# Optimization experiments

Hardware: AMD Instinct MI355X
Metric: run time of the kernel (lower is better)

Reference implementation:

```python
import jax, jax.numpy as jnp
import numpy as np

VOCAB, DIM, NC, KS, NCLASS = 50000, 300, 256, 3, 3
B, L1, L2 = 128, 512, 32
PAD = (KS - 1) // 2


def setup_inputs() -> dict:
    key = jax.random.key(0)
    ks = jax.random.split(key, 12)
    return {
        "context_ids": jax.random.randint(ks[0], (B, L1), 0, VOCAB),
        "context_masks": jnp.ones((B, L1), jnp.float32),
        "aspect_ids": jax.random.randint(ks[1], (B, L2), 0, VOCAB),
        "aspect_masks": jnp.ones((B, L2), jnp.float32),
        "wordmat": jax.random.normal(ks[2], (VOCAB, DIM), jnp.float32) * 0.1,
        "W": jax.random.normal(ks[3], (DIM, DIM), jnp.float32) * (2.0 / DIM) ** 0.5,
        "ctx_w": jax.random.normal(ks[4], (NC, DIM, KS), jnp.float32) * 0.02,
        "ctx_b": jnp.zeros((NC,), jnp.float32),
        "gate_w": jax.random.normal(ks[5], (NC, 2 * DIM, KS), jnp.float32) * 0.02,
        "gate_b": jnp.zeros((NC,), jnp.float32),
        "lin_w": jax.random.normal(ks[6], (NCLASS, NC), jnp.float32) * 0.05,
        "lin_b": jnp.zeros((NCLASS,), jnp.float32),
    }


def masked_softmax(A, mask):
    # A: (b, l1, l2); mask: (b, l2); normalize over dim=1 (l1), faithful to source
    A_max = jnp.max(A, axis=1, keepdims=True)
    A_exp = jnp.exp(A - A_max) * mask[:, None, :]
    return A_exp / (jnp.sum(A_exp, axis=1, keepdims=True) + 1e-10)


def conv1d(x, w, b):
    # x: (B, C_in, L), w: (C_out, C_in, K) -> (B, C_out, L)
    y = jax.lax.conv_general_dilated(x, w, (1,), [(PAD, PAD)],
                                     dimension_numbers=("NCH", "OIH", "NCH"))
    return y + b[None, :, None]


def reference(context_ids, context_masks, aspect_ids, aspect_masks,
              wordmat, W, ctx_w, ctx_b, gate_w, gate_b, lin_w, lin_b):
    context = wordmat[context_ids]          # (B, L1, D)
    aspect = wordmat[aspect_ids]            # (B, L2, D)
    # FullyAwareAttention
    sx = jax.nn.relu(jnp.einsum("bld,de->ble", context, W))
    sy = jax.nn.relu(jnp.einsum("bld,de->ble", aspect, W))
    s = jnp.einsum("bie,bje->bij", sx, sy)  # (B, L1, L2)
    alpha = masked_softmax(s, aspect_masks)
    att = jnp.einsum("bij,bjd->bid", alpha, aspect)  # (B, L1, D)
    gate_input = jnp.concatenate([context, att], axis=-1)  # (B, L1, 2D)
    sentiment = jnp.tanh(conv1d(context.transpose(0, 2, 1), ctx_w, ctx_b))
    gate = jax.nn.relu(conv1d(gate_input.transpose(0, 2, 1), gate_w, gate_b))
    out = jnp.max(sentiment * gate, axis=2)  # global maxpool over length
    return out @ lin_w.T + lin_b
```

## Files before the change

### kernel.cpp

```cpp
#include <hip/hip_runtime.h>
#include <hip/hip_bf16.h>
#include <math.h>
#include <stdint.h>

#define DIM 300
#define NC 256
#define KS 3
#define NCLASS 3
#define BB 128
#define L1 512
#define L2 32

#define XW 352
#define XROWS 514
#define ROW_B (XW * 2)
#define NKC 11
#define WP2_ELEMS (2 * 4 * 10 * 3 * 4 * 64 * 8)
#define WB_ELEMS (10 * 19 * 64 * 8)
#define WG2_ELEMS (3 * 10 * 16 * 64 * 8)
#define GT_ELEMS (BB * 3 * 32 * 256)
#define GP_ELEMS (BB * 2 * 2 * 3 * 4 * 64 * 8)
#define GP_B_STRIDE (2 * 2 * 3 * 4 * 64 * 8)
#define WAVE_WP_B (10 * 3 * 4 * 1024)

#define ABUF_B 4224
#define EP_LD 260

typedef __attribute__((ext_vector_type(8))) short bf16x8;
typedef __attribute__((ext_vector_type(4))) short bf16x4;
typedef __attribute__((ext_vector_type(4))) float f32x4;

#define GLOBAL_AS __attribute__((address_space(1)))
#define LDS_AS __attribute__((address_space(3)))

__device__ __forceinline__ void gload_lds16(const void* g, void* l) {
    __builtin_amdgcn_global_load_lds((const GLOBAL_AS void*)g, (LDS_AS void*)l, 16, 0, 0);
}

static __device__ __forceinline__ short bfr(float x) {
    __hip_bfloat16 h = __float2bfloat16(x);
    return *(short*)&h;
}

__global__ void prep_wp(const float* __restrict__ ctx_w,
                        const float* __restrict__ gate_w,
                        __hip_bfloat16* __restrict__ Wp2) {
    int idx = blockIdx.x * 256 + threadIdx.x;
    if (idx >= WP2_ELEMS) return;
    int jj = idx & 7;
    int lane = (idx >> 3) & 63;
    int n = (idx >> 9) & 3;
    int rest = idx >> 11;
    int tap = rest % 3;
    int r2 = rest / 3;
    int kc = r2 % 10;
    int w = r2 / 10;
    int role = w & 3, cbv = w >> 2;
    int k = kc * 32 + ((lane >> 4) << 3) + jj;
    int nl = role * 64 + n * 16 + (lane & 15);
    float v = 0.f;
    if (nl < 128) {
        int ch = cbv * 128 + nl;
        if (k < 300) v = ctx_w[(ch * DIM + k) * KS + tap];
    } else {
        int ch = cbv * 128 + (nl - 128);
        if (k < 300) v = gate_w[(ch * 2 * DIM + k) * KS + tap];
    }
    Wp2[idx] = __float2bfloat16(v);
}

__global__ void prep_wb(const float* __restrict__ Wm,
                        __hip_bfloat16* __restrict__ Wb) {
    int idx = blockIdx.x * 256 + threadIdx.x;
    if (idx >= WB_ELEMS) return;
    int j = idx & 7;
    int l = (idx >> 3) & 63;
    int r = idx >> 9;
    int nf = r % 19, kc = r / 19;
    int k = kc * 32 + ((l >> 4) << 3) + j;
    int n = nf * 16 + (l & 15);
    float v = (k < 300 && n < 300) ? Wm[k * DIM + n] : 0.f;
    Wb[idx] = __float2bfloat16(v);
}

__global__ void prep_wg2(const float* __restrict__ gate_w,
                         __hip_bfloat16* __restrict__ Wg2) {
    int idx = blockIdx.x * 256 + threadIdx.x;
    if (idx >= WG2_ELEMS) return;
    int jj = idx & 7;
    int lane = (idx >> 3) & 63;
    int rest = idx >> 9;
    int nf = rest % 16;
    int r2 = rest / 16;
    int kc = r2 % 10, tap = r2 / 10;
    int k = kc * 32 + ((lane >> 4) << 3) + jj;
    int n = nf * 16 + (lane & 15);
    float v = (k < 300) ? gate_w[(n * 2 * DIM + DIM + k) * KS + tap] : 0.f;
    Wg2[idx] = __float2bfloat16(v);
}

__global__ void gather_rows(const int* __restrict__ ids,
                            const float* __restrict__ wordmat,
                            __hip_bfloat16* __restrict__ aspb,
                            __hip_bfloat16* __restrict__ syb) {
    int row = blockIdx.x;
    int id = ids[row];
    const float* src = wordmat + (size_t)id * DIM;
    for (int d = threadIdx.x; d < 320; d += blockDim.x) {
        if (d < DIM) {
            aspb[(size_t)row * 320 + d] = __float2bfloat16(src[d]);
        } else {
            aspb[(size_t)row * 320 + d] = __float2bfloat16(0.f);
            if (d >= 304) syb[(size_t)row * 320 + d] = __float2bfloat16(0.f);
        }
    }
}

__global__ __launch_bounds__(256, 2) void prep_g(
        const __hip_bfloat16* __restrict__ aspb,
        const __hip_bfloat16* __restrict__ Wg2,
        __hip_bfloat16* __restrict__ Gt) {
    const int t = threadIdx.x, wave = t >> 6, l = t & 63;
    const int lane15 = l & 15, lq = l >> 4;
    const int b = blockIdx.x, tap = blockIdx.y;
    f32x4 acc[2][4];
    #pragma unroll
    for (int m = 0; m < 2; ++m)
        #pragma unroll
        for (int ni = 0; ni < 4; ++ni) acc[m][ni] = (f32x4)0.f;
    const char* Ab = (const char*)aspb + (size_t)b * 32 * 640;
    const bf16x8* WgV = (const bf16x8*)Wg2;
    for (int kc = 0; kc < 10; ++kc) {
        bf16x8 af[2];
        #pragma unroll
        for (int m = 0; m < 2; ++m)
            af[m] = *(const bf16x8*)(Ab + (size_t)(m * 16 + lane15) * 640 + kc * 64 + lq * 16);
        #pragma unroll
        for (int ni = 0; ni < 4; ++ni) {
            bf16x8 bw = WgV[((size_t)(tap * 10 + kc) * 16 + wave * 4 + ni) * 64 + l];
            #pragma unroll
            for (int m = 0; m < 2; ++m)
                acc[m][ni] = __builtin_amdgcn_mfma_f32_16x16x32_bf16(af[m], bw, acc[m][ni], 0, 0, 0);
        }
    }
    #pragma unroll
    for (int m = 0; m < 2; ++m)
        #pragma unroll
        for (int ni = 0; ni < 4; ++ni) {
            int c = (wave * 4 + ni) * 16 + lane15;
            #pragma unroll
            for (int i2 = 0; i2 < 4; ++i2) {
                int j = m * 16 + lq * 4 + i2;
                Gt[((size_t)(b * 3 + tap) * 32 + j) * 256 + c] = __float2bfloat16(acc[m][ni][i2]);
            }
        }
}

__global__ void prep_gp(const __hip_bfloat16* __restrict__ Gt,
                        __hip_bfloat16* __restrict__ Gp) {
    int idx = blockIdx.x * 256 + threadIdx.x;
    if (idx >= GP_ELEMS) return;
    int jj = idx & 7;
    int lane = (idx >> 3) & 63;
    int nf = (idx >> 9) & 3;
    int rest = idx >> 11;
    int tap = rest % 3;
    int r2 = rest / 3;
    int gr = r2 & 1, cbv = (r2 >> 1) & 1, b = r2 >> 2;
    int j = ((lane >> 4) << 3) + jj;
    int c = cbv * 128 + gr * 64 + nf * 16 + (lane & 15);
    Gp[idx] = Gt[((size_t)(b * 3 + tap) * 32 + j) * 256 + c];
}

__global__ __launch_bounds__(256) void xcat_x(const int* __restrict__ cids,
                                              const float* __restrict__ wordmat,
                                              __hip_bfloat16* __restrict__ Xc) {
    int t = threadIdx.x;
    int rloc = t >> 5, lane = t & 31;
    int row = blockIdx.x * 8 + rloc;
    int b = row >> 9, l = row & 511;
    size_t id = (size_t)cids[row];
    const float4* src = (const float4*)(wordmat + id * DIM);
    __hip_bfloat16* dst = Xc + ((size_t)b * XROWS + 1 + l) * XW;
    #pragma unroll
    for (int c = lane; c < 80; c += 32) {
        bf16x4 o;
        if (c < 75) {
            float4 f = src[c];
            o[0] = bfr(f.x); o[1] = bfr(f.y); o[2] = bfr(f.z); o[3] = bfr(f.w);
        } else {
            o = (bf16x4)0;
        }
        ((bf16x4*)dst)[c] = o;
    }
    if (blockIdx.x < 256 && t < 88) {
        int b2 = blockIdx.x >> 1;
        int gr = (blockIdx.x & 1) ? (XROWS - 1) : 0;
        ((bf16x4*)(Xc + ((size_t)b2 * XROWS + gr) * XW))[t] = (bf16x4)0;
    }
}

__global__ __launch_bounds__(256, 2) void sy_mfma(
        const __hip_bfloat16* __restrict__ aspb,
        const __hip_bfloat16* __restrict__ Wb,
        __hip_bfloat16* __restrict__ syb) {
    const int t = threadIdx.x, wave = t >> 6, l = t & 63;
    const int lane15 = l & 15, lq = l >> 4;
    const int g = blockIdx.x * 64 + wave * 16 + lane15;
    f32x4 acc[19];
    #pragma unroll
    for (int nf = 0; nf < 19; ++nf) acc[nf] = (f32x4)0.f;
    const bf16x8* Arow = (const bf16x8*)((const char*)aspb + (size_t)g * 640);
    const bf16x8* WbV = (const bf16x8*)Wb;
    for (int kc = 0; kc < 10; ++kc) {
        bf16x8 af = Arow[kc * 4 + lq];
        #pragma unroll
        for (int nf = 0; nf < 19; ++nf)
            acc[nf] = __builtin_amdgcn_mfma_f32_16x16x32_bf16(
                af, WbV[(kc * 19 + nf) * 64 + l], acc[nf], 0, 0, 0);
    }
    #pragma unroll
    for (int nf = 0; nf < 19; ++nf) {
        int col = nf * 16 + lane15;
        #pragma unroll
        for (int i2 = 0; i2 < 4; ++i2) {
            int row = blockIdx.x * 64 + wave * 16 + lq * 4 + i2;
            syb[(size_t)row * 320 + col] = __float2bfloat16(fmaxf(acc[nf][i2], 0.f));
        }
    }
}

__global__ __launch_bounds__(256, 2) void sxs_mfma(
        const __hip_bfloat16* __restrict__ Xc,
        const __hip_bfloat16* __restrict__ Wb,
        const __hip_bfloat16* __restrict__ syb,
        float* __restrict__ s) {
    __shared__ __align__(16) char sxL[4 * 16 * 640];
    const int t = threadIdx.x, wave = t >> 6, l = t & 63;
    const int lane15 = l & 15, lq = l >> 4;
    const int lb = blockIdx.x, b = blockIdx.y;
    const int g = b * XROWS + 1 + lb * 64 + wave * 16 + lane15;

    f32x4 acc[19];
    #pragma unroll
    for (int nf = 0; nf < 19; ++nf) acc[nf] = (f32x4)0.f;

    const bf16x8* Arow = (const bf16x8*)((const char*)Xc + (size_t)g * ROW_B);
    const bf16x8* WbV = (const bf16x8*)Wb;
    for (int kc = 0; kc < 10; ++kc) {
        bf16x8 af = Arow[kc * 4 + lq];
        #pragma unroll
        for (int nf = 0; nf < 19; ++nf)
            acc[nf] = __builtin_amdgcn_mfma_f32_16x16x32_bf16(
                af, WbV[(kc * 19 + nf) * 64 + l], acc[nf], 0, 0, 0);
    }

    char* sxW = sxL + wave * (16 * 640);
    if (l < 32) {
        int row = l >> 1;
        int phys = (2 + (l & 1)) ^ ((row >> 2) & 3);
        *(f32x4*)(sxW + row * 640 + 576 + phys * 16) = (f32x4)0.f;
    }
    #pragma unroll
    for (int nf = 0; nf < 19; ++nf) {
        int col = nf * 16 + lane15;
        #pragma unroll
        for (int i2 = 0; i2 < 4; ++i2) {
            int row = lq * 4 + i2;
            int off = row * 640 + ((col >> 5) << 6) +
                      ((((col >> 3) & 3) ^ ((row >> 2) & 3)) << 4) + ((col & 7) << 1);
            *(__hip_bfloat16*)(sxW + off) = __float2bfloat16(fmaxf(acc[nf][i2], 0.f));
        }
    }
    f32x4 acc2[2];
    acc2[0] = (f32x4)0.f;
    acc2[1] = (f32x4)0.f;
    const bf16x8* syV = (const bf16x8*)syb + (size_t)b * 32 * 40;
    for (int kc = 0; kc < 10; ++kc) {
        bf16x8 af2 = *(const bf16x8*)(sxW + lane15 * 640 + kc * 64 +
                                      ((lq ^ ((lane15 >> 2) & 3)) << 4));
        #pragma unroll
        for (int nj = 0; nj < 2; ++nj) {
            bf16x8 bfj = syV[(nj * 16 + lane15) * 40 + kc * 4 + lq];
            acc2[nj] = __builtin_amdgcn_mfma_f32_16x16x32_bf16(af2, bfj, acc2[nj], 0, 0, 0);
        }
    }
    #pragma unroll
    for (int nj = 0; nj < 2; ++nj)
        #pragma unroll
        for (int i2 = 0; i2 < 4; ++i2) {
            int i = lb * 64 + wave * 16 + lq * 4 + i2;
            s[((size_t)b * L1 + i) * L2 + nj * 16 + lane15] = acc2[nj][i2];
        }
}

__global__ __launch_bounds__(256) void softmax_col(const float* __restrict__ s,
                                                   const float* __restrict__ amask,
                                                   __hip_bfloat16* __restrict__ Xc) {
    __shared__ float red[256];
    __shared__ float cmax[16], cscale[16];
    int b = blockIdx.x, jh = blockIdx.y, t = threadIdx.x;
    int jl = t & 15, j = jh * 16 + jl, ii = t >> 4;
    const float* sb = s + (size_t)b * L1 * L2;
    float v[32];
    float m = -1e30f;
    #pragma unroll
    for (int q = 0; q < 32; ++q) {
        v[q] = sb[(size_t)(ii + q * 16) * L2 + j];
        m = fmaxf(m, v[q]);
    }
    red[t] = m;
    __syncthreads();
    if (t < 16) {
        float mm = red[t];
        for (int p = 1; p < 16; ++p) mm = fmaxf(mm, red[p * 16 + t]);
        cmax[t] = mm;
    }
    __syncthreads();
    float cm = cmax[jl];
    float sum = 0.f;
    #pragma unroll
    for (int q = 0; q < 32; ++q) {
        v[q] = expf(v[q] - cm);
        sum += v[q];
    }
    red[t] = sum;
    __syncthreads();
    if (t < 16) {
        float ss = 0.f;
        for (int p = 0; p < 16; ++p) ss += red[p * 16 + t];
        float mk = amask[b * L2 + jh * 16 + t];
        cscale[t] = mk / (mk * ss + 1e-10f);
    }
    __syncthreads();
    float sc = cscale[jl];
    #pragma unroll
    for (int q = 0; q < 32; ++q) {
        int row = ii + q * 16;
        Xc[((size_t)b * XROWS + 1 + row) * XW + 320 + j] = __float2bfloat16(v[q] * sc);
    }
}

__global__ __launch_bounds__(256, 4) void conv_mfma(
        const __hip_bfloat16* __restrict__ Xc,
        const __hip_bfloat16* __restrict__ Wp2,
        const __hip_bfloat16* __restrict__ Gp,
        const float* __restrict__ ctx_b,
        const float* __restrict__ gate_b,
        float* __restrict__ part) {
    __shared__ __align__(16) char lds[16 * EP_LD * 4];
    const int t = threadIdx.x, wave = t >> 6, lane = t & 63;
    const int lane15 = lane & 15, lq = lane >> 4;
    const int lb = blockIdx.x >> 1, cb = blockIdx.x & 1;
    const int b = blockIdx.y, l0 = lb * 64;
    const int role = wave ^ ((blockIdx.x & 1) << 1);

    f32x4 acc[4][4];
    #pragma unroll
    for (int m = 0; m < 4; ++m)
        #pragma unroll
        for (int n = 0; n < 4; ++n) acc[m][n] = (f32x4)0.f;

    const char* XcB = (const char*)Xc + ((size_t)b * XROWS + l0) * ROW_B;
    const char* bbase = (const char*)Wp2 + (size_t)(cb * 4 + role) * WAVE_WP_B + lane * 16;
    const char* gbase = (const char*)Gp + ((size_t)b * GP_B_STRIDE +
                        (size_t)(cb * 2 + (role & 1)) * (3 * 4 * 512)) * 2 + lane * 16;

    #define STAGE_A(kc_, buf_) do {                                              \
        char* Ab_ = lds + (buf_) * ABUF_B;                                       \
        _Pragma("unroll")                                                        \
        for (int i = 0; i < 2; ++i) {                                            \
            int chunk = (i * 4 + wave) * 64 + lane;                              \
            if (chunk < 264) {                                                   \
                int row_ = chunk >> 2, c_ = chunk & 3;                           \
                int sc_ = (c_ ^ ((row_ >> 1) & 3)) << 4;                         \
                gload_lds16(XcB + (size_t)row_ * ROW_B + (kc_) * 64 + sc_,       \
                            Ab_ + (i * 4 + wave) * 1024);                        \
            }                                                                    \
        }                                                                        \
    } while (0)

    STAGE_A(0, 0);
    __syncthreads();

    for (int kc = 0; kc < NKC; ++kc) {
        const int cbuf = kc & 1;
        if (kc < NKC - 1) STAGE_A(kc + 1, cbuf ^ 1);
        if (kc < 10 || role >= 2) {
            const char* Ab = lds + cbuf * ABUF_B;
            #pragma unroll
            for (int tap = 0; tap < 3; ++tap) {
                bf16x8 bw[4];
                #pragma unroll
                for (int n = 0; n < 4; ++n)
                    bw[n] = (kc < 10)
                        ? *(const bf16x8*)(bbase + (size_t)((kc * 3 + tap) * 4 + n) * 1024)
                        : *(const bf16x8*)(gbase + (size_t)(tap * 4 + n) * 1024);
                bf16x8 af[4];
                #pragma unroll
                for (int m = 0; m < 4; ++m) {
                    int row = m * 16 + lane15 + tap;
                    af[m] = *(const bf16x8*)(Ab + row * 64 +
                                             ((lq ^ ((row >> 1) & 3)) << 4));
                }
                #pragma unroll
                for (int m = 0; m < 4; ++m)
                    #pragma unroll
                    for (int n = 0; n < 4; ++n)
                        acc[m][n] = __builtin_amdgcn_mfma_f32_16x16x32_bf16(
                            af[m], bw[n], acc[m][n], 0, 0, 0);
            }
        }
        __syncthreads();
    }
    #undef STAGE_A

    const int c0 = cb * 128;
    const int cl = t & 127, rh = t >> 7;
    const float bs = ctx_b[c0 + cl];
    const float bg = gate_b[c0 + cl];
    float* ep = (float*)lds;
    float pm = -1e30f;
    for (int ms = 0; ms < 4; ++ms) {
        __syncthreads();
        #pragma unroll
        for (int n = 0; n < 4; ++n) {
            int col = (role << 6) + (n << 4) + lane15;
            #pragma unroll
            for (int i2 = 0; i2 < 4; ++i2)
                ep[(lq * 4 + i2) * EP_LD + col] = acc[ms][n][i2];
        }
        __syncthreads();
        #pragma unroll
        for (int rr = 0; rr < 8; ++rr) {
            int r = rh * 8 + rr;
            float sv = ep[r * EP_LD + cl] + bs;
            float gv = ep[r * EP_LD + 128 + cl] + bg;
            pm = fmaxf(pm, tanhf(sv) * fmaxf(gv, 0.f));
        }
    }
    __syncthreads();
    ep[t] = pm;
    __syncthreads();
    if (t < 128)
        part[((size_t)b * 8 + lb) * 256 + c0 + cl] = fmaxf(ep[t], ep[t + 128]);
}

__global__ __launch_bounds__(256) void finalize(const float* __restrict__ part,
                                                const float* __restrict__ lin_w,
                                                const float* __restrict__ lin_b,
                                                float* __restrict__ out) {
    __shared__ float pl[256];
    __shared__ float red[256];
    int b = blockIdx.x, t = threadIdx.x;
    float p = part[((size_t)b * 8) * 256 + t];
    for (int lb = 1; lb < 8; ++lb)
        p = fmaxf(p, part[((size_t)b * 8 + lb) * 256 + t]);
    pl[t] = p;
    __syncthreads();
    for (int n = 0; n < NCLASS; ++n) {
        red[t] = pl[t] * lin_w[n * NC + t];
        __syncthreads();
        for (int sft = 128; sft > 0; sft >>= 1) {
            if (t < sft) red[t] += red[t + sft];
            __syncthreads();
        }
        if (t == 0) out[b * NCLASS + n] = red[0] + lin_b[n];
        __syncthreads();
    }
}

extern "C" void kernel_launch(void* const* d_in, const int* in_sizes, int n_in,
                              void* d_out, int out_size, void* d_ws, size_t ws_size,
                              hipStream_t stream) {
    const int* cids = (const int*)d_in[0];
    const int* aids = (const int*)d_in[2];
    const float* amask = (const float*)d_in[3];
    const float* wordmat = (const float*)d_in[4];
    const float* Wm = (const float*)d_in[5];
    const float* ctx_w = (const float*)d_in[6];
    const float* ctx_b = (const float*)d_in[7];
    const float* gate_w = (const float*)d_in[8];
    const float* gate_b = (const float*)d_in[9];
    const float* lin_w = (const float*)d_in[10];
    const float* lin_b = (const float*)d_in[11];
    float* out = (float*)d_out;

    float* sbuf = (float*)d_ws;
    float* part = sbuf + 2097152;
    __hip_bfloat16* aspb = (__hip_bfloat16*)(part + 262144);
    __hip_bfloat16* sybf = aspb + 1310720;
    __hip_bfloat16* Wb   = sybf + 1310720;
    __hip_bfloat16* Wp2  = Wb + WB_ELEMS;
    __hip_bfloat16* Wg2  = Wp2 + WP2_ELEMS;
    __hip_bfloat16* Gt   = Wg2 + WG2_ELEMS;
    __hip_bfloat16* Gp   = Gt + GT_ELEMS;
    __hip_bfloat16* Xc   = Gp + GP_ELEMS;

    prep_wp<<<(WP2_ELEMS + 255) / 256, 256, 0, stream>>>(ctx_w, gate_w, Wp2);
    prep_wb<<<(WB_ELEMS + 255) / 256, 256, 0, stream>>>(Wm, Wb);
    prep_wg2<<<(WG2_ELEMS + 255) / 256, 256, 0, stream>>>(gate_w, Wg2);
    gather_rows<<<BB * L2, 256, 0, stream>>>(aids, wordmat, aspb, sybf);
    xcat_x<<<BB * L1 / 8, 256, 0, stream>>>(cids, wordmat, Xc);
    sy_mfma<<<(BB * L2) / 64, 256, 0, stream>>>(aspb, Wb, sybf);
    prep_g<<<dim3(BB, 3), 256, 0, stream>>>(aspb, Wg2, Gt);
    prep_gp<<<(GP_ELEMS + 255) / 256, 256, 0, stream>>>(Gt, Gp);
    sxs_mfma<<<dim3(L1 / 64, BB), 256, 0, stream>>>(Xc, Wb, sybf, sbuf);
    softmax_col<<<dim3(BB, 2), 256, 0, stream>>>(sbuf, amask, Xc);
    conv_mfma<<<dim3(16, BB), 256, 0, stream>>>(Xc, Wp2, Gp, ctx_b, gate_b, part);
    finalize<<<BB, 256, 0, stream>>>(part, lin_w, lin_b, out);
}
```

Before: 195.5 us.

## Merge prep kernels, drop Gp repack, widen conv blocks to 512 threads

Folds the three weight-prep kernels and the aspect gather into one launch, and merges the sy projection and the G precompute into one kernel. The Gp repack kernel is removed; the gate waves now read Gt directly with scalar 2-byte gathers. Conv blocks become 512 threads covering all 256 channels, so each staged X tile is shared by both channel halves. Softmax is split over 4 column groups for more parallelism. These changes cut launch overhead and duplicated X loads, at the cost of uncoalesced Gt reads and higher per-block register and LDS pressure.

New measurement: 171.6 us. 1.14x faster.

```diff
diff --git a/kernel.cpp b/kernel.cpp
--- a/kernel.cpp
+++ b/kernel.cpp
@@ -19,12 +19,11 @@
 #define WB_ELEMS (10 * 19 * 64 * 8)
 #define WG2_ELEMS (3 * 10 * 16 * 64 * 8)
 #define GT_ELEMS (BB * 3 * 32 * 256)
-#define GP_ELEMS (BB * 2 * 2 * 3 * 4 * 64 * 8)
-#define GP_B_STRIDE (2 * 2 * 3 * 4 * 64 * 8)
+#define GATH_ELEMS (BB * L2 * 320)
 #define WAVE_WP_B (10 * 3 * 4 * 1024)
 
 #define ABUF_B 4224
-#define EP_LD 260
+#define EP_LD 516
 
 typedef __attribute__((ext_vector_type(8))) short bf16x8;
 typedef __attribute__((ext_vector_type(4))) short bf16x4;
@@ -42,134 +41,76 @@
     return *(short*)&h;
 }
 
-__global__ void prep_wp(const float* __restrict__ ctx_w,
-                        const float* __restrict__ gate_w,
-                        __hip_bfloat16* __restrict__ Wp2) {
+__global__ void prep_all(const float* __restrict__ ctx_w,
+                         const float* __restrict__ gate_w,
+                         const float* __restrict__ Wm,
+                         const int* __restrict__ aids,
+                         const float* __restrict__ wordmat,
+                         __hip_bfloat16* __restrict__ Wp2,
+                         __hip_bfloat16* __restrict__ Wb,
+                         __hip_bfloat16* __restrict__ Wg2,
+                         __hip_bfloat16* __restrict__ aspb,
+                         __hip_bfloat16* __restrict__ syb) {
     int idx = blockIdx.x * 256 + threadIdx.x;
-    if (idx >= WP2_ELEMS) return;
-    int jj = idx & 7;
-    int lane = (idx >> 3) & 63;
-    int n = (idx >> 9) & 3;
-    int rest = idx >> 11;
-    int tap = rest % 3;
-    int r2 = rest / 3;
-    int kc = r2 % 10;
-    int w = r2 / 10;
-    int role = w & 3, cbv = w >> 2;
-    int k = kc * 32 + ((lane >> 4) << 3) + jj;
-    int nl = role * 64 + n * 16 + (lane & 15);
-    float v = 0.f;
-    if (nl < 128) {
-        int ch = cbv * 128 + nl;
-        if (k < 300) v = ctx_w[(ch * DIM + k) * KS + tap];
-    } else {
-        int ch = cbv * 128 + (nl - 128);
-        if (k < 300) v = gate_w[(ch * 2 * DIM + k) * KS + tap];
-    }
-    Wp2[idx] = __float2bfloat16(v);
-}
-
-__global__ void prep_wb(const float* __restrict__ Wm,
-                        __hip_bfloat16* __restrict__ Wb) {
-    int idx = blockIdx.x * 256 + threadIdx.x;
-    if (idx >= WB_ELEMS) return;
-    int j = idx & 7;
-    int l = (idx >> 3) & 63;
-    int r = idx >> 9;
-    int nf = r % 19, kc = r / 19;
-    int k = kc * 32 + ((l >> 4) << 3) + j;
-    int n = nf * 16 + (l & 15);
-    float v = (k < 300 && n < 300) ? Wm[k * DIM + n] : 0.f;
-    Wb[idx] = __float2bfloat16(v);
-}
-
-__global__ void prep_wg2(const float* __restrict__ gate_w,
-                         __hip_bfloat16* __restrict__ Wg2) {
-    int idx = blockIdx.x * 256 + threadIdx.x;
-    if (idx >= WG2_ELEMS) return;
-    int jj = idx & 7;
-    int lane = (idx >> 3) & 63;
-    int rest = idx >> 9;
-    int nf = rest % 16;
-    int r2 = rest / 16;
-    int kc = r2 % 10, tap = r2 / 10;
-    int k = kc * 32 + ((lane >> 4) << 3) + jj;
-    int n = nf * 16 + (lane & 15);
-    float v = (k < 300) ? gate_w[(n * 2 * DIM + DIM + k) * KS + tap] : 0.f;
-    Wg2[idx] = __float2bfloat16(v);
-}
-
-__global__ void gather_rows(const int* __restrict__ ids,
-                            const float* __restrict__ wordmat,
-                            __hip_bfloat16* __restrict__ aspb,
-                            __hip_bfloat16* __restrict__ syb) {
-    int row = blockIdx.x;
-    int id = ids[row];
-    const float* src = wordmat + (size_t)id * DIM;
-    for (int d = threadIdx.x; d < 320; d += blockDim.x) {
+    if (idx < WP2_ELEMS) {
+        int jj = idx & 7;
+        int lane = (idx >> 3) & 63;
+        int n = (idx >> 9) & 3;
+        int rest = idx >> 11;
+        int tap = rest % 3;
+        int r2 = rest / 3;
+        int kc = r2 % 10;
+        int w = r2 / 10;
+        int role = w & 3, cbv = w >> 2;
+        int k = kc * 32 + ((lane >> 4) << 3) + jj;
+        int nl = role * 64 + n * 16 + (lane & 15);
+        float v = 0.f;
+        if (nl < 128) {
+            int ch = cbv * 128 + nl;
+            if (k < 300) v = ctx_w[(ch * DIM + k) * KS + tap];
+        } else {
+            int ch = cbv * 128 + (nl - 128);
+            if (k < 300) v = gate_w[(ch * 2 * DIM + k) * KS + tap];
+        }
+        Wp2[idx] = __float2bfloat16(v);
+        return;
+    }
+    idx -= WP2_ELEMS;
+    if (idx < WB_ELEMS) {
+        int j = idx & 7;
+        int l = (idx >> 3) & 63;
+        int r = idx >> 9;
+        int nf = r % 19, kc = r / 19;
+        int k = kc * 32 + ((l >> 4) << 3) + j;
+        int n = nf * 16 + (l & 15);
+        float v = (k < 300 && n < 300) ? Wm[k * DIM + n] : 0.f;
+        Wb[idx] = __float2bfloat16(v);
+        return;
+    }
+    idx -= WB_ELEMS;
+    if (idx < WG2_ELEMS) {
+        int jj = idx & 7;
+        int lane = (idx >> 3) & 63;
+        int rest = idx >> 9;
+        int nf = rest % 16;
+        int r2 = rest / 16;
+        int kc = r2 % 10, tap = r2 / 10;
+        int k = kc * 32 + ((lane >> 4) << 3) + jj;
+        int n = nf * 16 + (lane & 15);
+        float v = (k < 300) ? gate_w[(n * 2 * DIM + DIM + k) * KS + tap] : 0.f;
+        Wg2[idx] = __float2bfloat16(v);
+        return;
+    }
+    idx -= WG2_ELEMS;
+    if (idx < GATH_ELEMS) {
+        int row = idx / 320, d = idx - row * 320;
         if (d < DIM) {
-            aspb[(size_t)row * 320 + d] = __float2bfloat16(src[d]);
+            aspb[(size_t)row * 320 + d] = __float2bfloat16(wordmat[(size_t)aids[row] * DIM + d]);
         } else {
             aspb[(size_t)row * 320 + d] = __float2bfloat16(0.f);
             if (d >= 304) syb[(size_t)row * 320 + d] = __float2bfloat16(0.f);
         }
     }
-}
-
-__global__ __launch_bounds__(256, 2) void prep_g(
-        const __hip_bfloat16* __restrict__ aspb,
-        const __hip_bfloat16* __restrict__ Wg2,
-        __hip_bfloat16* __restrict__ Gt) {
-    const int t = threadIdx.x, wave = t >> 6, l = t & 63;
-    const int lane15 = l & 15, lq = l >> 4;
-    const int b = blockIdx.x, tap = blockIdx.y;
-    f32x4 acc[2][4];
-    #pragma unroll
-    for (int m = 0; m < 2; ++m)
-        #pragma unroll
-        for (int ni = 0; ni < 4; ++ni) acc[m][ni] = (f32x4)0.f;
-    const char* Ab = (const char*)aspb + (size_t)b * 32 * 640;
-    const bf16x8* WgV = (const bf16x8*)Wg2;
-    for (int kc = 0; kc < 10; ++kc) {
-        bf16x8 af[2];
-        #pragma unroll
-        for (int m = 0; m < 2; ++m)
-            af[m] = *(const bf16x8*)(Ab + (size_t)(m * 16 + lane15) * 640 + kc * 64 + lq * 16);
-        #pragma unroll
-        for (int ni = 0; ni < 4; ++ni) {
-            bf16x8 bw = WgV[((size_t)(tap * 10 + kc) * 16 + wave * 4 + ni) * 64 + l];
-            #pragma unroll
-            for (int m = 0; m < 2; ++m)
-                acc[m][ni] = __builtin_amdgcn_mfma_f32_16x16x32_bf16(af[m], bw, acc[m][ni], 0, 0, 0);
-        }
-    }
-    #pragma unroll
-    for (int m = 0; m < 2; ++m)
-        #pragma unroll
-        for (int ni = 0; ni < 4; ++ni) {
-            int c = (wave * 4 + ni) * 16 + lane15;
-            #pragma unroll
-            for (int i2 = 0; i2 < 4; ++i2) {
-                int j = m * 16 + lq * 4 + i2;
-                Gt[((size_t)(b * 3 + tap) * 32 + j) * 256 + c] = __float2bfloat16(acc[m][ni][i2]);
-            }
-        }
-}
-
-__global__ void prep_gp(const __hip_bfloat16* __restrict__ Gt,
-                        __hip_bfloat16* __restrict__ Gp) {
-    int idx = blockIdx.x * 256 + threadIdx.x;
-    if (idx >= GP_ELEMS) return;
-    int jj = idx & 7;
-    int lane = (idx >> 3) & 63;
-    int nf = (idx >> 9) & 3;
-    int rest = idx >> 11;
-    int tap = rest % 3;
-    int r2 = rest / 3;
-    int gr = r2 & 1, cbv = (r2 >> 1) & 1, b = r2 >> 2;
-    int j = ((lane >> 4) << 3) + jj;
-    int c = cbv * 128 + gr * 64 + nf * 16 + (lane & 15);
-    Gp[idx] = Gt[((size_t)(b * 3 + tap) * 32 + j) * 256 + c];
 }
 
 __global__ __launch_bounds__(256) void xcat_x(const int* __restrict__ cids,
@@ -200,33 +141,71 @@
     }
 }
 
-__global__ __launch_bounds__(256, 2) void sy_mfma(
+__global__ __launch_bounds__(256, 2) void asp_mfma(
         const __hip_bfloat16* __restrict__ aspb,
         const __hip_bfloat16* __restrict__ Wb,
-        __hip_bfloat16* __restrict__ syb) {
+        const __hip_bfloat16* __restrict__ Wg2,
+        __hip_bfloat16* __restrict__ syb,
+        __hip_bfloat16* __restrict__ Gt) {
     const int t = threadIdx.x, wave = t >> 6, l = t & 63;
     const int lane15 = l & 15, lq = l >> 4;
-    const int g = blockIdx.x * 64 + wave * 16 + lane15;
-    f32x4 acc[19];
-    #pragma unroll
-    for (int nf = 0; nf < 19; ++nf) acc[nf] = (f32x4)0.f;
-    const bf16x8* Arow = (const bf16x8*)((const char*)aspb + (size_t)g * 640);
-    const bf16x8* WbV = (const bf16x8*)Wb;
-    for (int kc = 0; kc < 10; ++kc) {
-        bf16x8 af = Arow[kc * 4 + lq];
-        #pragma unroll
-        for (int nf = 0; nf < 19; ++nf)
-            acc[nf] = __builtin_amdgcn_mfma_f32_16x16x32_bf16(
-                af, WbV[(kc * 19 + nf) * 64 + l], acc[nf], 0, 0, 0);
-    }
-    #pragma unroll
-    for (int nf = 0; nf < 19; ++nf) {
-        int col = nf * 16 + lane15;
-        #pragma unroll
-        for (int i2 = 0; i2 < 4; ++i2) {
-            int row = blockIdx.x * 64 + wave * 16 + lq * 4 + i2;
-            syb[(size_t)row * 320 + col] = __float2bfloat16(fmaxf(acc[nf][i2], 0.f));
-        }
+    if (blockIdx.x < 64) {
+        const int g = blockIdx.x * 64 + wave * 16 + lane15;
+        f32x4 acc[19];
+        #pragma unroll
+        for (int nf = 0; nf < 19; ++nf) acc[nf] = (f32x4)0.f;
+        const bf16x8* Arow = (const bf16x8*)((const char*)aspb + (size_t)g * 640);
+        const bf16x8* WbV = (const bf16x8*)Wb;
+        for (int kc = 0; kc < 10; ++kc) {
+            bf16x8 af = Arow[kc * 4 + lq];
+            #pragma unroll
+            for (int nf = 0; nf < 19; ++nf)
+                acc[nf] = __builtin_amdgcn_mfma_f32_16x16x32_bf16(
+                    af, WbV[(kc * 19 + nf) * 64 + l], acc[nf], 0, 0, 0);
+        }
+        #pragma unroll
+        for (int nf = 0; nf < 19; ++nf) {
+            int col = nf * 16 + lane15;
+            #pragma unroll
+            for (int i2 = 0; i2 < 4; ++i2) {
+                int row = blockIdx.x * 64 + wave * 16 + lq * 4 + i2;
+                syb[(size_t)row * 320 + col] = __float2bfloat16(fmaxf(acc[nf][i2], 0.f));
+            }
+        }
+    } else {
+        const int i = blockIdx.x - 64;
+        const int b = i / 3, tap = i - b * 3;
+        f32x4 acc[2][4];
+        #pragma unroll
+        for (int m = 0; m < 2; ++m)
+            #pragma unroll
+            for (int ni = 0; ni < 4; ++ni) acc[m][ni] = (f32x4)0.f;
+        const char* Ab = (const char*)aspb + (size_t)b * 32 * 640;
+        const bf16x8* WgV = (const bf16x8*)Wg2;
+        for (int kc = 0; kc < 10; ++kc) {
+            bf16x8 af[2];
+            #pragma unroll
+            for (int m = 0; m < 2; ++m)
+                af[m] = *(const bf16x8*)(Ab + (size_t)(m * 16 + lane15) * 640 + kc * 64 + lq * 16);
+            #pragma unroll
+            for (int ni = 0; ni < 4; ++ni) {
+                bf16x8 bw = WgV[((size_t)(tap * 10 + kc) * 16 + wave * 4 + ni) * 64 + l];
+                #pragma unroll
+                for (int m = 0; m < 2; ++m)
+                    acc[m][ni] = __builtin_amdgcn_mfma_f32_16x16x32_bf16(af[m], bw, acc[m][ni], 0, 0, 0);
+            }
+        }
+        #pragma unroll
+        for (int m = 0; m < 2; ++m)
+            #pragma unroll
+            for (int ni = 0; ni < 4; ++ni) {
+                int c = (wave * 4 + ni) * 16 + lane15;
+                #pragma unroll
+                for (int i2 = 0; i2 < 4; ++i2) {
+                    int j = m * 16 + lq * 4 + i2;
+                    Gt[((size_t)(b * 3 + tap) * 32 + j) * 256 + c] = __float2bfloat16(acc[m][ni][i2]);
+                }
+            }
     }
 }
 
@@ -298,62 +277,64 @@
                                                    const float* __restrict__ amask,
                                                    __hip_bfloat16* __restrict__ Xc) {
     __shared__ float red[256];
-    __shared__ float cmax[16], cscale[16];
+    __shared__ float cmax[8], cscale[8];
     int b = blockIdx.x, jh = blockIdx.y, t = threadIdx.x;
-    int jl = t & 15, j = jh * 16 + jl, ii = t >> 4;
+    int jl = t & 7, j = jh * 8 + jl, ii = t >> 3;
     const float* sb = s + (size_t)b * L1 * L2;
-    float v[32];
+    float v[16];
     float m = -1e30f;
     #pragma unroll
-    for (int q = 0; q < 32; ++q) {
-        v[q] = sb[(size_t)(ii + q * 16) * L2 + j];
+    for (int q = 0; q < 16; ++q) {
+        v[q] = sb[(size_t)(ii + q * 32) * L2 + j];
         m = fmaxf(m, v[q]);
     }
     red[t] = m;
     __syncthreads();
-    if (t < 16) {
+    if (t < 8) {
         float mm = red[t];
-        for (int p = 1; p < 16; ++p) mm = fmaxf(mm, red[p * 16 + t]);
+        for (int p = 1; p < 32; ++p) mm = fmaxf(mm, red[p * 8 + t]);
         cmax[t] = mm;
     }
     __syncthreads();
     float cm = cmax[jl];
     float sum = 0.f;
     #pragma unroll
-    for (int q = 0; q < 32; ++q) {
+    for (int q = 0; q < 16; ++q) {
         v[q] = expf(v[q] - cm);
         sum += v[q];
     }
     red[t] = sum;
     __syncthreads();
-    if (t < 16) {
+    if (t < 8) {
         float ss = 0.f;
-        for (int p = 0; p < 16; ++p) ss += red[p * 16 + t];
-        float mk = amask[b * L2 + jh * 16 + t];
+        for (int p = 0; p < 32; ++p) ss += red[p * 8 + t];
+        float mk = amask[b * L2 + jh * 8 + t];
         cscale[t] = mk / (mk * ss + 1e-10f);
     }
     __syncthreads();
     float sc = cscale[jl];
     #pragma unroll
-    for (int q = 0; q < 32; ++q) {
-        int row = ii + q * 16;
+    for (int q = 0; q < 16; ++q) {
+        int row = ii + q * 32;
         Xc[((size_t)b * XROWS + 1 + row) * XW + 320 + j] = __float2bfloat16(v[q] * sc);
     }
 }
 
-__global__ __launch_bounds__(256, 4) void conv_mfma(
+__global__ __launch_bounds__(512, 4) void conv_mfma(
         const __hip_bfloat16* __restrict__ Xc,
         const __hip_bfloat16* __restrict__ Wp2,
-        const __hip_bfloat16* __restrict__ Gp,
+        const __hip_bfloat16* __restrict__ Gt,
         const float* __restrict__ ctx_b,
         const float* __restrict__ gate_b,
         float* __restrict__ part) {
     __shared__ __align__(16) char lds[16 * EP_LD * 4];
     const int t = threadIdx.x, wave = t >> 6, lane = t & 63;
     const int lane15 = lane & 15, lq = lane >> 4;
-    const int lb = blockIdx.x >> 1, cb = blockIdx.x & 1;
-    const int b = blockIdx.y, l0 = lb * 64;
-    const int role = wave ^ ((blockIdx.x & 1) << 1);
+    const int lb = blockIdx.x, b = blockIdx.y, l0 = lb * 64;
+    const bool isGate = wave >= 4;
+    const int u = isGate ? wave - 4 : wave;
+    const int cbv = u >> 1;
+    const int role = isGate ? 2 + (u & 1) : (u & 1);
 
     f32x4 acc[4][4];
     #pragma unroll
@@ -362,21 +343,16 @@
         for (int n = 0; n < 4; ++n) acc[m][n] = (f32x4)0.f;
 
     const char* XcB = (const char*)Xc + ((size_t)b * XROWS + l0) * ROW_B;
-    const char* bbase = (const char*)Wp2 + (size_t)(cb * 4 + role) * WAVE_WP_B + lane * 16;
-    const char* gbase = (const char*)Gp + ((size_t)b * GP_B_STRIDE +
-                        (size_t)(cb * 2 + (role & 1)) * (3 * 4 * 512)) * 2 + lane * 16;
+    const char* bbase = (const char*)Wp2 + (size_t)(cbv * 4 + role) * WAVE_WP_B + lane * 16;
 
     #define STAGE_A(kc_, buf_) do {                                              \
         char* Ab_ = lds + (buf_) * ABUF_B;                                       \
-        _Pragma("unroll")                                                        \
-        for (int i = 0; i < 2; ++i) {                                            \
-            int chunk = (i * 4 + wave) * 64 + lane;                              \
-            if (chunk < 264) {                                                   \
-                int row_ = chunk >> 2, c_ = chunk & 3;                           \
-                int sc_ = (c_ ^ ((row_ >> 1) & 3)) << 4;                         \
-                gload_lds16(XcB + (size_t)row_ * ROW_B + (kc_) * 64 + sc_,       \
-                            Ab_ + (i * 4 + wave) * 1024);                        \
-            }                                                                    \
+        int chunk = wave * 64 + lane;                                            \
+        if (chunk < 264) {                                                       \
+            int row_ = chunk >> 2, c_ = chunk & 3;                               \
+            int sc_ = (c_ ^ ((row_ >> 1) & 3)) << 4;                             \
+            gload_lds16(XcB + (size_t)row_ * ROW_B + (kc_) * 64 + sc_,           \
+                        Ab_ + wave * 1024);                                      \
         }                                                                        \
     } while (0)
 
@@ -386,22 +362,19 @@
     for (int kc = 0; kc < NKC; ++kc) {
         const int cbuf = kc & 1;
         if (kc < NKC - 1) STAGE_A(kc + 1, cbuf ^ 1);
-        if (kc < 10 || role >= 2) {
-            const char* Ab = lds + cbuf * ABUF_B;
+        const char* Ab = lds + cbuf * ABUF_B;
+        if (kc < 10) {
             #pragma unroll
             for (int tap = 0; tap < 3; ++tap) {
                 bf16x8 bw[4];
                 #pragma unroll
                 for (int n = 0; n < 4; ++n)
-                    bw[n] = (kc < 10)
-                        ? *(const bf16x8*)(bbase + (size_t)((kc * 3 + tap) * 4 + n) * 1024)
-                        : *(const bf16x8*)(gbase + (size_t)(tap * 4 + n) * 1024);
+                    bw[n] = *(const bf16x8*)(bbase + (size_t)((kc * 3 + tap) * 4 + n) * 1024);
                 bf16x8 af[4];
                 #pragma unroll
                 for (int m = 0; m < 4; ++m) {
                     int row = m * 16 + lane15 + tap;
-                    af[m] = *(const bf16x8*)(Ab + row * 64 +
-                                             ((lq ^ ((row >> 1) & 3)) << 4));
+                    af[m] = *(const bf16x8*)(Ab + row * 64 + ((lq ^ ((row >> 1) & 3)) << 4));
                 }
                 #pragma unroll
                 for (int m = 0; m < 4; ++m)
@@ -410,22 +383,49 @@
                         acc[m][n] = __builtin_amdgcn_mfma_f32_16x16x32_bf16(
                             af[m], bw[n], acc[m][n], 0, 0, 0);
             }
+        } else if (isGate) {
+            const char* GtB = (const char*)Gt + (size_t)b * 3 * (32 * 256 * 2);
+            #pragma unroll
+            for (int tap = 0; tap < 3; ++tap) {
+                bf16x8 bw[4];
+                #pragma unroll
+                for (int n = 0; n < 4; ++n) {
+                    #pragma unroll
+                    for (int jj = 0; jj < 8; ++jj)
+                        ((short*)&bw[n])[jj] = *(const short*)(GtB +
+                            (size_t)tap * (32 * 256 * 2) +
+                            (size_t)(lq * 8 + jj) * 512 +
+                            (size_t)(u * 64 + n * 16 + lane15) * 2);
+                }
+                bf16x8 af[4];
+                #pragma unroll
+                for (int m = 0; m < 4; ++m) {
+                    int row = m * 16 + lane15 + tap;
+                    af[m] = *(const bf16x8*)(Ab + row * 64 + ((lq ^ ((row >> 1) & 3)) << 4));
+                }
+                #pragma unroll
+                for (int m = 0; m < 4; ++m)
+                    #pragma unroll
+                    for (int n = 0; n < 4; ++n)
+                        acc[m][n] = __builtin_amdgcn_mfma_f32_16x16x32_bf16(
+                            af[m], bw[n], acc[m][n], 0, 0, 0);
+            }
         }
         __syncthreads();
     }
     #undef STAGE_A
 
-    const int c0 = cb * 128;
-    const int cl = t & 127, rh = t >> 7;
-    const float bs = ctx_b[c0 + cl];
-    const float bg = gate_b[c0 + cl];
+    const int cl = t & 255, rh = t >> 8;
+    const float bs = ctx_b[cl];
+    const float bg = gate_b[cl];
+    const int colbase = (isGate ? 256 + u * 64 : u * 64);
     float* ep = (float*)lds;
     float pm = -1e30f;
     for (int ms = 0; ms < 4; ++ms) {
         __syncthreads();
         #pragma unroll
         for (int n = 0; n < 4; ++n) {
-            int col = (role << 6) + (n << 4) + lane15;
+            int col = colbase + (n << 4) + lane15;
             #pragma unroll
             for (int i2 = 0; i2 < 4; ++i2)
                 ep[(lq * 4 + i2) * EP_LD + col] = acc[ms][n][i2];
@@ -435,15 +435,15 @@
         for (int rr = 0; rr < 8; ++rr) {
             int r = rh * 8 + rr;
             float sv = ep[r * EP_LD + cl] + bs;
-            float gv = ep[r * EP_LD + 128 + cl] + bg;
+            float gv = ep[r * EP_LD + 256 + cl] + bg;
             pm = fmaxf(pm, tanhf(sv) * fmaxf(gv, 0.f));
         }
     }
     __syncthreads();
     ep[t] = pm;
     __syncthreads();
-    if (t < 128)
-        part[((size_t)b * 8 + lb) * 256 + c0 + cl] = fmaxf(ep[t], ep[t + 128]);
+    if (t < 256)
+        part[((size_t)b * 8 + lb) * 256 + t] = fmaxf(ep[t], ep[t + 256]);
 }
 
 __global__ __launch_bounds__(256) void finalize(const float* __restrict__ part,
@@ -494,19 +494,15 @@
     __hip_bfloat16* Wp2  = Wb + WB_ELEMS;
     __hip_bfloat16* Wg2  = Wp2 + WP2_ELEMS;
     __hip_bfloat16* Gt   = Wg2 + WG2_ELEMS;
-    __hip_bfloat16* Gp   = Gt + GT_ELEMS;
-    __hip_bfloat16* Xc   = Gp + GP_ELEMS;
-
-    prep_wp<<<(WP2_ELEMS + 255) / 256, 256, 0, stream>>>(ctx_w, gate_w, Wp2);
-    prep_wb<<<(WB_ELEMS + 255) / 256, 256, 0, stream>>>(Wm, Wb);
-    prep_wg2<<<(WG2_ELEMS + 255) / 256, 256, 0, stream>>>(gate_w, Wg2);
-    gather_rows<<<BB * L2, 256, 0, stream>>>(aids, wordmat, aspb, sybf);
+    __hip_bfloat16* Xc   = Gt + GT_ELEMS;
+
+    const int prepN = WP2_ELEMS + WB_ELEMS + WG2_ELEMS + GATH_ELEMS;
+    prep_all<<<(prepN + 255) / 256, 256, 0, stream>>>(ctx_w, gate_w, Wm, aids, wordmat,
+                                                      Wp2, Wb, Wg2, aspb, sybf);
     xcat_x<<<BB * L1 / 8, 256, 0, stream>>>(cids, wordmat, Xc);
-    sy_mfma<<<(BB * L2) / 64, 256, 0, stream>>>(aspb, Wb, sybf);
-    prep_g<<<dim3(BB, 3), 256, 0, stream>>>(aspb, Wg2, Gt);
-    prep_gp<<<(GP_ELEMS + 255) / 256, 256, 0, stream>>>(Gt, Gp);
+    asp_mfma<<<64 + BB * 3, 256, 0, stream>>>(aspb, Wb, Wg2, sybf, Gt);
     sxs_mfma<<<dim3(L1 / 64, BB), 256, 0, stream>>>(Xc, Wb, sybf, sbuf);
-    softmax_col<<<dim3(BB, 2), 256, 0, stream>>>(sbuf, amask, Xc);
-    conv_mfma<<<dim3(16, BB), 256, 0, stream>>>(Xc, Wp2, Gp, ctx_b, gate_b, part);
+    softmax_col<<<dim3(BB, 4), 256, 0, stream>>>(sbuf, amask, Xc);
+    conv_mfma<<<dim3(8, BB), 512, 0, stream>>>(Xc, Wp2, Gt, ctx_b, gate_b, part);
     finalize<<<BB, 256, 0, stream>>>(part, lin_w, lin_b, out);
 }
```
